# Optimization experiments

Measured on AMD Instinct MI355X. Metric: run time of the kernel, lower is better.

Reference implementation:

```python
import jax, jax.numpy as jnp
import numpy as np

S, B, E, H = 2048, 4, 512, 8
HD = E // H


def setup_inputs() -> dict:
    key = jax.random.key(0)
    ks = jax.random.split(key, 5)
    scale = 1.0 / np.sqrt(E)
    return {
        "query": jax.random.normal(ks[0], (S, B, E), jnp.float32),
        "key": jax.random.normal(ks[1], (S, B, E), jnp.float32),
        "value": jax.random.normal(ks[2], (S, B, E), jnp.float32),
        "in_proj_weight": jax.random.normal(ks[3], (3 * E, E), jnp.float32) * scale,
        "in_proj_bias": jnp.zeros((3 * E,), jnp.float32),
        "out_proj_weight": jax.random.normal(ks[4], (E, E), jnp.float32) * scale,
        "out_proj_bias": jnp.zeros((E,), jnp.float32),
    }


def reference(query, key, value, in_proj_weight, in_proj_bias, out_proj_weight, out_proj_bias):
    tgt_len, bsz, embed_dim = query.shape
    src_len = key.shape[0]
    # Quirk of this module: first chunk (w_qk) projects BOTH q and k; third chunk projects v.
    w_qk = in_proj_weight[:embed_dim]
    w_v = in_proj_weight[2 * embed_dim:]
    b_qk = in_proj_bias[:embed_dim]
    b_v = in_proj_bias[2 * embed_dim:]
    q = query @ w_qk.T + b_qk          # [S, B, E]
    k = key @ w_qk.T + b_qk
    v = value @ w_v.T + b_v
    # (S, B, E) -> (B*H, S, HD)
    def split_heads(x, n):
        return x.reshape(n, bsz * H, HD).transpose(1, 0, 2)
    q = split_heads(q, tgt_len) / jnp.sqrt(jnp.asarray(HD, q.dtype))
    k = split_heads(k, src_len)
    v = split_heads(v, src_len)
    scores = jnp.einsum("bqd,bkd->bqk", q, k)          # [B*H, S, S] full score matrix
    attn = jax.nn.softmax(scores, axis=-1)
    out = jnp.einsum("bqk,bkd->bqd", attn, v)          # [B*H, S, HD]
    out = out.transpose(1, 0, 2).reshape(tgt_len * bsz, embed_dim)
    out = out @ out_proj_weight.T + out_proj_bias
    return out.reshape(tgt_len, bsz, embed_dim)
```

## Files before the change

### kernel.cpp

```cpp
#include <hip/hip_runtime.h>
#include <hip/hip_bf16.h>

typedef __attribute__((ext_vector_type(8))) short s16x8;
typedef __attribute__((ext_vector_type(4))) short s16x4;
typedef __attribute__((ext_vector_type(4))) float f32x4;

#if __has_builtin(__builtin_amdgcn_exp2f)
#define EXP2F(x) __builtin_amdgcn_exp2f(x)
#else
#define EXP2F(x) exp2f(x)
#endif

#define EMB   512
#define MROWS 8192

__device__ __forceinline__ short f2bf(float f) {
    union { float f; unsigned u; } z; z.f = f;
    unsigned r = z.u + 0x7FFF + ((z.u >> 16) & 1);
    return (short)(r >> 16);
}
__device__ __forceinline__ short f2bf_fast(float f) {
    union { float f; unsigned u; } z; z.f = f;
    return (short)((z.u + 0x8000u) >> 16);
}
__device__ __forceinline__ short f2bf_cvt(float f) {
    union { __hip_bfloat16 h; short s; } cv;
    cv.h = __float2bfloat16(f);
    return cv.s;
}
__device__ __forceinline__ int swzs(int s) { return s ^ ((s >> 3) & 7); }

__device__ __forceinline__ void barrier_fast() {
    asm volatile("s_waitcnt lgkmcnt(0)" ::: "memory");
    __builtin_amdgcn_s_barrier();
    __builtin_amdgcn_sched_barrier(0);
}

__global__ __launch_bounds__(256) void w_to_bf16(const float* __restrict__ W,
                                                 short* __restrict__ wb, int n)
{
    int i = (blockIdx.x * 256 + threadIdx.x) * 8;
    if (i < n) {
        f32x4 a = *(const f32x4*)(W + i);
        f32x4 b = *(const f32x4*)(W + i + 4);
        s16x8 o;
        o[0] = f2bf(a[0]); o[1] = f2bf(a[1]); o[2] = f2bf(a[2]); o[3] = f2bf(a[3]);
        o[4] = f2bf(b[0]); o[5] = f2bf(b[1]); o[6] = f2bf(b[2]); o[7] = f2bf(b[3]);
        *(s16x8*)(wb + i) = o;
    }
}

template<int AF32, int BF32>
__device__ __forceinline__ void gemm_mainloop(const void* __restrict__ Ag,
                                              const void* __restrict__ Bg,
                                              short* sA, short* sB,
                                              f32x4 acc[2][4], int K)
{
    const int tid  = threadIdx.x;
    const int lane = tid & 63;
    const int wv   = tid >> 6;
    const int lsw  = lane ^ ((lane >> 3) & 7);
    const int amt  = (wv >> 1) * 2;
    const int bnt  = (wv & 1) * 4;

    const int srow = tid >> 3, qd = tid & 7;
    const int offL = (qd >> 2) * 4096
                   + swzs((srow >> 4) * 64 + (qd & 3) * 16 + (srow & 15)) * 8;
    const int offH = (qd >> 2) * 4096
                   + swzs(((srow >> 4) + 4) * 64 + (qd & 3) * 16 + (srow & 15)) * 8;

    f32x4 aF0[4], aF1[4], bF0[4], bF1[4];
    s16x8 aH0[2], aH1[2], bH0[2], bH1[2];

    auto loadX = [&](const void* G, int kt, f32x4 fr[4], s16x8 hr[2], int F32) {
        if (F32) {
            const float* g = (const float*)G + (size_t)srow * K + kt + qd * 8;
            fr[0] = *(const f32x4*)g;
            fr[1] = *(const f32x4*)(g + 4);
            fr[2] = *(const f32x4*)(g + (size_t)64 * K);
            fr[3] = *(const f32x4*)(g + (size_t)64 * K + 4);
        } else {
            const short* g = (const short*)G + (size_t)srow * K + kt + qd * 8;
            hr[0] = *(const s16x8*)g;
            hr[1] = *(const s16x8*)(g + (size_t)64 * K);
        }
    };
    auto commitX = [&](short* s, f32x4 fr[4], s16x8 hr[2], int F32) {
        if (F32) {
            s16x8 o;
            o[0] = f2bf_fast(fr[0][0]); o[1] = f2bf_fast(fr[0][1]);
            o[2] = f2bf_fast(fr[0][2]); o[3] = f2bf_fast(fr[0][3]);
            o[4] = f2bf_fast(fr[1][0]); o[5] = f2bf_fast(fr[1][1]);
            o[6] = f2bf_fast(fr[1][2]); o[7] = f2bf_fast(fr[1][3]);
            *(s16x8*)(s + offL) = o;
            o[0] = f2bf_fast(fr[2][0]); o[1] = f2bf_fast(fr[2][1]);
            o[2] = f2bf_fast(fr[2][2]); o[3] = f2bf_fast(fr[2][3]);
            o[4] = f2bf_fast(fr[3][0]); o[5] = f2bf_fast(fr[3][1]);
            o[6] = f2bf_fast(fr[3][2]); o[7] = f2bf_fast(fr[3][3]);
            *(s16x8*)(s + offH) = o;
        } else {
            *(s16x8*)(s + offL) = hr[0];
            *(s16x8*)(s + offH) = hr[1];
        }
    };
    auto compute = [&](const short* sAc, const short* sBc) {
#pragma unroll
        for (int h = 0; h < 2; ++h) {
            s16x8 a[2], b[4];
#pragma unroll
            for (int i = 0; i < 2; ++i)
                a[i] = *(const s16x8*)(sAc + h * 4096 + ((amt + i) * 64 + lsw) * 8);
#pragma unroll
            for (int j = 0; j < 4; ++j)
                b[j] = *(const s16x8*)(sBc + h * 4096 + ((bnt + j) * 64 + lsw) * 8);
#pragma unroll
            for (int i = 0; i < 2; ++i)
#pragma unroll
                for (int j = 0; j < 4; ++j)
                    acc[i][j] = __builtin_amdgcn_mfma_f32_16x16x32_bf16(a[i], b[j], acc[i][j], 0, 0, 0);
        }
    };

    loadX(Ag, 0, aF0, aH0, AF32);  loadX(Bg, 0, bF0, bH0, BF32);
    loadX(Ag, 64, aF1, aH1, AF32); loadX(Bg, 64, bF1, bH1, BF32);
    commitX(sA, aF0, aH0, AF32); commitX(sB, bF0, bH0, BF32);
    barrier_fast();

    for (int kt = 0; kt < K; kt += 128) {
        const int k2 = (kt + 128 < K) ? kt + 128 : 0;
        loadX(Ag, k2, aF0, aH0, AF32); loadX(Bg, k2, bF0, bH0, BF32);
        compute(sA, sB);
        commitX(sA + 8192, aF1, aH1, AF32); commitX(sB + 8192, bF1, bH1, BF32);
        barrier_fast();
        const int k3 = (kt + 192 < K) ? kt + 192 : 0;
        loadX(Ag, k3, aF1, aH1, AF32); loadX(Bg, k3, bF1, bH1, BF32);
        compute(sA + 8192, sB + 8192);
        commitX(sA, aF0, aH0, AF32); commitX(sB, bF0, bH0, BF32);
        barrier_fast();
    }
}

__global__ __launch_bounds__(512, 4) void qkv_proj(const float* __restrict__ query,
                                                   const float* __restrict__ key,
                                                   const float* __restrict__ value,
                                                   const short* __restrict__ wb,
                                                   const float* __restrict__ bias,
                                                   short* __restrict__ q,
                                                   short* __restrict__ k,
                                                   short* __restrict__ vt)
{
    __shared__ __align__(16) short smem[32768];
    short* sA = smem;
    short* sB = smem + 16384;

    const int z = blockIdx.z;
    const float* X  = (z == 0) ? query : (z == 1) ? key : value;
    const short* Wz = wb   + (z == 2 ? (size_t)1024 * EMB : 0);
    const float* bz = bias + (z == 2 ? 1024 : 0);
    const float scale = (z == 0) ? 0.125f * 1.44269504f : 1.0f;

    const int blockM = blockIdx.x * 128, blockN = blockIdx.y * 128;

    f32x4 acc[2][4];
#pragma unroll
    for (int i = 0; i < 2; ++i)
#pragma unroll
        for (int j = 0; j < 4; ++j)
            acc[i][j] = (f32x4){0.f, 0.f, 0.f, 0.f};

    gemm_mainloop<1, 0>(X + (size_t)blockM * EMB, Wz + (size_t)blockN * EMB,
                        sA, sB, acc, EMB);

    const int tid = threadIdx.x, lane = tid & 63, wv = tid >> 6;
    const int l15 = lane & 15, quad = lane >> 4;
    const int wm = (wv >> 1) * 32, wn = (wv & 1) * 64;

#pragma unroll
    for (int j = 0; j < 4; ++j) {
        int colL = wn + j * 16 + l15;
        float bval = bz[blockN + colL];
        int hL = colL >> 6, hd = colL & 63;
#pragma unroll
        for (int i = 0; i < 2; ++i) {
#pragma unroll
            for (int r = 0; r < 4; ++r) {
                int rowL = wm + i * 16 + quad * 4 + r;
                int b = rowL & 3, sp = rowL >> 2;
                float val = (acc[i][j][r] + bval) * scale;
                int idx;
                if (z == 2) {
                    int R = (b * 2 + hL) * 64 + hd;
                    idx = R * 32 + (((sp >> 3) ^ (R & 3)) << 3) + (sp & 7);
                } else {
                    idx = ((b * 2 + hL) * 32 + sp) * 64 + hd;
                }
                smem[idx] = f2bf(val);
            }
        }
    }
    barrier_fast();

    if (z == 2) {
        int R = tid;
        int b = tid >> 7, hL = (tid >> 6) & 1, hd = tid & 63;
        int h = (blockN >> 6) + hL;
        short* dst = vt + ((size_t)(b * 8 + h) * 64 + hd) * 2048 + (blockM >> 2);
#pragma unroll
        for (int u = 0; u < 4; ++u)
            ((s16x8*)dst)[u] = *(const s16x8*)(smem + R * 32 + ((u ^ (R & 3)) << 3));
    } else {
        const s16x8* src = (const s16x8*)(smem + tid * 32);
        int b = tid >> 7, hL = (tid >> 6) & 1;
        int sp = (tid >> 1) & 31, hdh = (tid & 1) * 32;
        int h = (blockN >> 6) + hL;
        short* dstp = (z == 0) ? q : k;
        short* dst = dstp + ((size_t)(b * 8 + h) * 2048 + (blockM >> 2) + sp) * 64 + hdh;
#pragma unroll
        for (int u = 0; u < 4; ++u) ((s16x8*)dst)[u] = src[u];
    }
}

__global__ __launch_bounds__(256, 2) void flash_attn(const short* __restrict__ q,
                                                     const short* __restrict__ k,
                                                     const short* __restrict__ vt,
                                                     short* __restrict__ attn)
{
    __shared__ __align__(16) short sK[2][8192];
    __shared__ __align__(16) short sV[2][8192];
    const int bh = blockIdx.x;
    const int q0 = blockIdx.y * 128;
    const int tid = threadIdx.x, wv = tid >> 6, lane = tid & 63;
    const int l15 = lane & 15, quad = lane >> 4;
    const int lsw = lane ^ ((lane >> 3) & 7);

    s16x8 qf[2][2];
#pragma unroll
    for (int qr = 0; qr < 2; ++qr) {
        const short* qp = q + ((size_t)(bh * 2048 + q0 + wv * 32 + qr * 16 + l15)) * 64 + quad * 8;
        qf[qr][0] = *(const s16x8*)qp;
        qf[qr][1] = *(const s16x8*)(qp + 32);
    }

    const short* kg = k  + (size_t)bh * 2048 * 64;
    const short* vg = vt + (size_t)bh * 64 * 2048;

    const int rk = tid >> 2, qd = tid & 3;
    const int pr = (rk & 35) | ((rk & 24) >> 1) | ((rk & 4) << 2);
    const int kw0 = swzs((pr >> 4) * 64 + qd * 16 + (pr & 15)) * 8;
    const int vw0 = swzs((rk >> 4) * 64 + qd * 16 + (rk & 15)) * 8;
    const short* kgt = kg + (size_t)rk * 64 + qd * 8;
    const short* vgt = vg + (size_t)rk * 2048 + qd * 8;

    f32x4 o[2][4];
    float ls[2][4];
#pragma unroll
    for (int qr = 0; qr < 2; ++qr)
#pragma unroll
        for (int i = 0; i < 4; ++i) { o[qr][i] = (f32x4){0.f, 0.f, 0.f, 0.f}; ls[qr][i] = 0.f; }

    s16x8 kr[2][2], vr[2][2];
    auto loadT = [&](int kt) {
#pragma unroll
        for (int s = 0; s < 2; ++s) {
            kr[s][0] = *(const s16x8*)(kgt + (size_t)(kt + s * 64) * 64);
            kr[s][1] = *(const s16x8*)(kgt + (size_t)(kt + s * 64) * 64 + 32);
            vr[s][0] = *(const s16x8*)(vgt + kt + s * 64);
            vr[s][1] = *(const s16x8*)(vgt + kt + s * 64 + 32);
        }
    };
    auto commitT = [&](int buf) {
#pragma unroll
        for (int s = 0; s < 2; ++s) {
            *(s16x8*)(sK[buf] + s * 4096 + kw0)        = kr[s][0];
            *(s16x8*)(sK[buf] + s * 4096 + kw0 + 2048) = kr[s][1];
            *(s16x8*)(sV[buf] + s * 4096 + vw0)        = vr[s][0];
            *(s16x8*)(sV[buf] + s * 4096 + vw0 + 2048) = vr[s][1];
        }
    };
    auto computeQK = [&](const short* Kc, f32x4 sc[2][4]) {
#pragma unroll
        for (int ct = 0; ct < 4; ++ct) {
            s16x8 kf0 = *(const s16x8*)(Kc + (ct * 64 + lsw) * 8);
            s16x8 kf1 = *(const s16x8*)(Kc + (ct * 64 + lsw) * 8 + 2048);
#pragma unroll
            for (int qr = 0; qr < 2; ++qr) {
                f32x4 c = (f32x4){0.f, 0.f, 0.f, 0.f};
                c = __builtin_amdgcn_mfma_f32_16x16x32_bf16(kf0, qf[qr][0], c, 0, 0, 0);
                c = __builtin_amdgcn_mfma_f32_16x16x32_bf16(kf1, qf[qr][1], c, 0, 0, 0);
                sc[qr][ct] = c;
            }
        }
    };
    auto softmaxPV = [&](f32x4 sc[2][4], const short* Vc) {
        s16x8 pf[2][2];
#pragma unroll
        for (int qr = 0; qr < 2; ++qr)
#pragma unroll
            for (int c = 0; c < 2; ++c)
#pragma unroll
                for (int h = 0; h < 2; ++h)
#pragma unroll
                    for (int r = 0; r < 4; ++r) {
                        float p = EXP2F(sc[qr][2 * c + h][r]);
                        ls[qr][r] += p;
                        pf[qr][c][h * 4 + r] = f2bf_cvt(p);
                    }
#pragma unroll
        for (int nt = 0; nt < 4; ++nt)
#pragma unroll
            for (int c = 0; c < 2; ++c) {
                s16x8 vf = *(const s16x8*)(Vc + ((c * 4 + nt) * 64 + lsw) * 8);
#pragma unroll
                for (int qr = 0; qr < 2; ++qr)
                    o[qr][nt] = __builtin_amdgcn_mfma_f32_16x16x32_bf16(pf[qr][c], vf, o[qr][nt], 0, 0, 0);
            }
    };

    loadT(0);
    commitT(0);
    __syncthreads();

    int cur = 0;
    for (int kt = 0; kt < 2048; kt += 128) {
        loadT((kt + 128) & 2047);

        f32x4 sc0[2][4], sc1[2][4];
        computeQK(sK[cur], sc0);
        computeQK(sK[cur] + 4096, sc1);
        softmaxPV(sc0, sV[cur]);
        softmaxPV(sc1, sV[cur] + 4096);

        commitT(cur ^ 1);
        __syncthreads();
        cur ^= 1;
    }

    const int b = bh >> 3, h = bh & 7;
#pragma unroll
    for (int qr = 0; qr < 2; ++qr) {
        float s = ls[qr][0] + ls[qr][1] + ls[qr][2] + ls[qr][3];
        s += __shfl_xor(s, 16, 64);
        s += __shfl_xor(s, 32, 64);
        float sinv = 1.0f / s;
        float inv[4];
#pragma unroll
        for (int r = 0; r < 4; ++r)
            inv[r] = __shfl(sinv, quad * 20 + r, 64);
#pragma unroll
        for (int r = 0; r < 4; ++r) {
            int srow = q0 + wv * 32 + qr * 16 + quad * 4 + r;
#pragma unroll
            for (int nt = 0; nt < 4; ++nt)
                attn[(size_t)(srow * 4 + b) * 512 + h * 64 + nt * 16 + l15] = f2bf(o[qr][nt][r] * inv[r]);
        }
    }
}

__global__ __launch_bounds__(512, 4) void out_proj(const short* __restrict__ attn,
                                                   const float* __restrict__ W,
                                                   const float* __restrict__ bias,
                                                   float* __restrict__ out)
{
    __shared__ __align__(16) short smem[32768];
    short* sA = smem;
    short* sB = smem + 16384;
    const int blockM = blockIdx.x * 128, blockN = blockIdx.y * 128;

    f32x4 acc[2][4];
#pragma unroll
    for (int i = 0; i < 2; ++i)
#pragma unroll
        for (int j = 0; j < 4; ++j)
            acc[i][j] = (f32x4){0.f, 0.f, 0.f, 0.f};

    gemm_mainloop<0, 1>(attn + (size_t)blockM * EMB, W + (size_t)blockN * EMB,
                        sA, sB, acc, EMB);

    const int tid = threadIdx.x, lane = tid & 63, wv = tid >> 6;
    const int l15 = lane & 15, quad = lane >> 4;
    const int wm = (wv >> 1) * 32, wn = (wv & 1) * 64;

#pragma unroll
    for (int j = 0; j < 4; ++j) {
        int col = blockN + wn + j * 16 + l15;
        float bval = bias[col];
#pragma unroll
        for (int i = 0; i < 2; ++i) {
#pragma unroll
            for (int r = 0; r < 4; ++r) {
                int row = blockM + wm + i * 16 + quad * 4 + r;
                out[(size_t)row * 512 + col] = acc[i][j][r] + bval;
            }
        }
    }
}

extern "C" void kernel_launch(void* const* d_in, const int* in_sizes, int n_in,
                              void* d_out, int out_size, void* d_ws, size_t ws_size,
                              hipStream_t stream)
{
    const float* query = (const float*)d_in[0];
    const float* key   = (const float*)d_in[1];
    const float* value = (const float*)d_in[2];
    const float* ipw   = (const float*)d_in[3];
    const float* ipb   = (const float*)d_in[4];
    const float* opw   = (const float*)d_in[5];
    const float* opb   = (const float*)d_in[6];
    float* out = (float*)d_out;

    const size_t NELEM = (size_t)MROWS * EMB;
    short* q    = (short*)d_ws;
    short* k    = q + NELEM;
    short* attn = k + NELEM;
    short* vt   = (short*)d_out;
    short* wb   = (short*)d_out + NELEM;

    w_to_bf16 <<<dim3(384),      256, 0, stream>>>(ipw, wb, 1536 * EMB);
    qkv_proj  <<<dim3(64, 4, 3), 512, 0, stream>>>(query, key, value, wb, ipb, q, k, vt);
    flash_attn<<<dim3(32, 16),   256, 0, stream>>>(q, k, vt, attn);
    out_proj  <<<dim3(64, 4),    512, 0, stream>>>(attn, opw, opb, out);
}
```

Before: 174.9 us.

## Double flash-attention block size and split-K the output projection with a reduce pass

Result: slower. 186.2 us (+6.5%).

```diff
diff --git a/kernel.cpp b/kernel.cpp
--- a/kernel.cpp
+++ b/kernel.cpp
@@ -54,7 +54,7 @@
 __device__ __forceinline__ void gemm_mainloop(const void* __restrict__ Ag,
                                               const void* __restrict__ Bg,
                                               short* sA, short* sB,
-                                              f32x4 acc[2][4], int K)
+                                              f32x4 acc[2][4], int ld, int Klen)
 {
     const int tid  = threadIdx.x;
     const int lane = tid & 63;
@@ -74,15 +74,15 @@
 
     auto loadX = [&](const void* G, int kt, f32x4 fr[4], s16x8 hr[2], int F32) {
         if (F32) {
-            const float* g = (const float*)G + (size_t)srow * K + kt + qd * 8;
+            const float* g = (const float*)G + (size_t)srow * ld + kt + qd * 8;
             fr[0] = *(const f32x4*)g;
             fr[1] = *(const f32x4*)(g + 4);
-            fr[2] = *(const f32x4*)(g + (size_t)64 * K);
-            fr[3] = *(const f32x4*)(g + (size_t)64 * K + 4);
+            fr[2] = *(const f32x4*)(g + (size_t)64 * ld);
+            fr[3] = *(const f32x4*)(g + (size_t)64 * ld + 4);
         } else {
-            const short* g = (const short*)G + (size_t)srow * K + kt + qd * 8;
+            const short* g = (const short*)G + (size_t)srow * ld + kt + qd * 8;
             hr[0] = *(const s16x8*)g;
-            hr[1] = *(const s16x8*)(g + (size_t)64 * K);
+            hr[1] = *(const s16x8*)(g + (size_t)64 * ld);
         }
     };
     auto commitX = [&](short* s, f32x4 fr[4], s16x8 hr[2], int F32) {
@@ -126,13 +126,13 @@
     commitX(sA, aF0, aH0, AF32); commitX(sB, bF0, bH0, BF32);
     barrier_fast();
 
-    for (int kt = 0; kt < K; kt += 128) {
-        const int k2 = (kt + 128 < K) ? kt + 128 : 0;
+    for (int kt = 0; kt < Klen; kt += 128) {
+        const int k2 = (kt + 128 < Klen) ? kt + 128 : 0;
         loadX(Ag, k2, aF0, aH0, AF32); loadX(Bg, k2, bF0, bH0, BF32);
         compute(sA, sB);
         commitX(sA + 8192, aF1, aH1, AF32); commitX(sB + 8192, bF1, bH1, BF32);
         barrier_fast();
-        const int k3 = (kt + 192 < K) ? kt + 192 : 0;
+        const int k3 = (kt + 192 < Klen) ? kt + 192 : 0;
         loadX(Ag, k3, aF1, aH1, AF32); loadX(Bg, k3, bF1, bH1, BF32);
         compute(sA + 8192, sB + 8192);
         commitX(sA, aF0, aH0, AF32); commitX(sB, bF0, bH0, BF32);
@@ -169,7 +169,7 @@
             acc[i][j] = (f32x4){0.f, 0.f, 0.f, 0.f};
 
     gemm_mainloop<1, 0>(X + (size_t)blockM * EMB, Wz + (size_t)blockN * EMB,
-                        sA, sB, acc, EMB);
+                        sA, sB, acc, EMB, EMB);
 
     const int tid = threadIdx.x, lane = tid & 63, wv = tid >> 6;
     const int l15 = lane & 15, quad = lane >> 4;
@@ -220,7 +220,7 @@
     }
 }
 
-__global__ __launch_bounds__(256, 2) void flash_attn(const short* __restrict__ q,
+__global__ __launch_bounds__(512, 2) void flash_attn(const short* __restrict__ q,
                                                      const short* __restrict__ k,
                                                      const short* __restrict__ vt,
                                                      short* __restrict__ attn)
@@ -228,7 +228,7 @@
     __shared__ __align__(16) short sK[2][8192];
     __shared__ __align__(16) short sV[2][8192];
     const int bh = blockIdx.x;
-    const int q0 = blockIdx.y * 128;
+    const int q0 = blockIdx.y * 256;
     const int tid = threadIdx.x, wv = tid >> 6, lane = tid & 63;
     const int l15 = lane & 15, quad = lane >> 4;
     const int lsw = lane ^ ((lane >> 3) & 7);
@@ -244,12 +244,13 @@
     const short* kg = k  + (size_t)bh * 2048 * 64;
     const short* vg = vt + (size_t)bh * 64 * 2048;
 
-    const int rk = tid >> 2, qd = tid & 3;
+    const int tL = tid & 255, sub = tid >> 8;
+    const int rk = tL >> 2, qd = tL & 3;
     const int pr = (rk & 35) | ((rk & 24) >> 1) | ((rk & 4) << 2);
-    const int kw0 = swzs((pr >> 4) * 64 + qd * 16 + (pr & 15)) * 8;
-    const int vw0 = swzs((rk >> 4) * 64 + qd * 16 + (rk & 15)) * 8;
-    const short* kgt = kg + (size_t)rk * 64 + qd * 8;
-    const short* vgt = vg + (size_t)rk * 2048 + qd * 8;
+    const int kw0 = sub * 4096 + swzs((pr >> 4) * 64 + qd * 16 + (pr & 15)) * 8;
+    const int vw0 = sub * 4096 + swzs((rk >> 4) * 64 + qd * 16 + (rk & 15)) * 8;
+    const short* kgt = kg + (size_t)(sub * 64 + rk) * 64 + qd * 8;
+    const short* vgt = vg + (size_t)rk * 2048 + sub * 64 + qd * 8;
 
     f32x4 o[2][4];
     float ls[2][4];
@@ -258,24 +259,18 @@
 #pragma unroll
         for (int i = 0; i < 4; ++i) { o[qr][i] = (f32x4){0.f, 0.f, 0.f, 0.f}; ls[qr][i] = 0.f; }
 
-    s16x8 kr[2][2], vr[2][2];
+    s16x8 kA, kB, vA, vB;
     auto loadT = [&](int kt) {
-#pragma unroll
-        for (int s = 0; s < 2; ++s) {
-            kr[s][0] = *(const s16x8*)(kgt + (size_t)(kt + s * 64) * 64);
-            kr[s][1] = *(const s16x8*)(kgt + (size_t)(kt + s * 64) * 64 + 32);
-            vr[s][0] = *(const s16x8*)(vgt + kt + s * 64);
-            vr[s][1] = *(const s16x8*)(vgt + kt + s * 64 + 32);
-        }
+        kA = *(const s16x8*)(kgt + (size_t)kt * 64);
+        kB = *(const s16x8*)(kgt + (size_t)kt * 64 + 32);
+        vA = *(const s16x8*)(vgt + kt);
+        vB = *(const s16x8*)(vgt + kt + 32);
     };
     auto commitT = [&](int buf) {
-#pragma unroll
-        for (int s = 0; s < 2; ++s) {
-            *(s16x8*)(sK[buf] + s * 4096 + kw0)        = kr[s][0];
-            *(s16x8*)(sK[buf] + s * 4096 + kw0 + 2048) = kr[s][1];
-            *(s16x8*)(sV[buf] + s * 4096 + vw0)        = vr[s][0];
-            *(s16x8*)(sV[buf] + s * 4096 + vw0 + 2048) = vr[s][1];
-        }
+        *(s16x8*)(sK[buf] + kw0)        = kA;
+        *(s16x8*)(sK[buf] + kw0 + 2048) = kB;
+        *(s16x8*)(sV[buf] + vw0)        = vA;
+        *(s16x8*)(sV[buf] + vw0 + 2048) = vB;
     };
     auto computeQK = [&](const short* Kc, f32x4 sc[2][4]) {
 #pragma unroll
@@ -356,15 +351,17 @@
     }
 }
 
-__global__ __launch_bounds__(512, 4) void out_proj(const short* __restrict__ attn,
-                                                   const float* __restrict__ W,
-                                                   const float* __restrict__ bias,
-                                                   float* __restrict__ out)
+__global__ __launch_bounds__(512, 4) void out_proj_k(const short* __restrict__ attn,
+                                                     const float* __restrict__ W,
+                                                     const float* __restrict__ bias,
+                                                     float* __restrict__ out,
+                                                     float* __restrict__ pbuf)
 {
     __shared__ __align__(16) short smem[32768];
     short* sA = smem;
     short* sB = smem + 16384;
     const int blockM = blockIdx.x * 128, blockN = blockIdx.y * 128;
+    const int split = blockIdx.z;
 
     f32x4 acc[2][4];
 #pragma unroll
@@ -373,25 +370,40 @@
         for (int j = 0; j < 4; ++j)
             acc[i][j] = (f32x4){0.f, 0.f, 0.f, 0.f};
 
-    gemm_mainloop<0, 1>(attn + (size_t)blockM * EMB, W + (size_t)blockN * EMB,
-                        sA, sB, acc, EMB);
+    gemm_mainloop<0, 1>(attn + (size_t)blockM * EMB + split * 256,
+                        W    + (size_t)blockN * EMB + split * 256,
+                        sA, sB, acc, EMB, 256);
 
     const int tid = threadIdx.x, lane = tid & 63, wv = tid >> 6;
     const int l15 = lane & 15, quad = lane >> 4;
     const int wm = (wv >> 1) * 32, wn = (wv & 1) * 64;
+    float* dst = split ? out : pbuf;
 
 #pragma unroll
     for (int j = 0; j < 4; ++j) {
         int col = blockN + wn + j * 16 + l15;
-        float bval = bias[col];
+        float bval = split ? bias[col] : 0.f;
 #pragma unroll
         for (int i = 0; i < 2; ++i) {
 #pragma unroll
             for (int r = 0; r < 4; ++r) {
                 int row = blockM + wm + i * 16 + quad * 4 + r;
-                out[(size_t)row * 512 + col] = acc[i][j][r] + bval;
+                dst[(size_t)row * 512 + col] = acc[i][j][r] + bval;
             }
         }
+    }
+}
+
+__global__ __launch_bounds__(256) void reduce_add(float* __restrict__ out,
+                                                  const float* __restrict__ pbuf)
+{
+    int i = (blockIdx.x * 256 + threadIdx.x) * 16;
+#pragma unroll
+    for (int u = 0; u < 4; ++u) {
+        f32x4 a = *(const f32x4*)(out + i + u * 4);
+        f32x4 b = *(const f32x4*)(pbuf + i + u * 4);
+        a[0] += b[0]; a[1] += b[1]; a[2] += b[2]; a[3] += b[3];
+        *(f32x4*)(out + i + u * 4) = a;
     }
 }
 
@@ -414,9 +426,11 @@
     short* attn = k + NELEM;
     short* vt   = (short*)d_out;
     short* wb   = (short*)d_out + NELEM;
+    float* pbuf = (float*)d_ws;
 
     w_to_bf16 <<<dim3(384),      256, 0, stream>>>(ipw, wb, 1536 * EMB);
     qkv_proj  <<<dim3(64, 4, 3), 512, 0, stream>>>(query, key, value, wb, ipb, q, k, vt);
-    flash_attn<<<dim3(32, 16),   256, 0, stream>>>(q, k, vt, attn);
-    out_proj  <<<dim3(64, 4),    512, 0, stream>>>(attn, opw, opb, out);
-}
+    flash_attn<<<dim3(32, 8),    512, 0, stream>>>(q, k, vt, attn);
+    out_proj_k<<<dim3(64, 4, 2), 512, 0, stream>>>(attn, opw, opb, out, pbuf);
+    reduce_add<<<dim3(1024),     256, 0, stream>>>(out, pbuf);
+}
```
